# Kernel tuning notes

Hardware: AMD Instinct MI355X
Metric: run time of the kernel (lower is better)

The kernel has to match this reference:

```python
import jax, jax.numpy as jnp
import numpy as np

T, IN_SZ, OUT_SZ = 512, 1024, 1024
INIT_TAU = 2.0   # sig_tau = sigmoid(init_tau) is the leak factor
V_TH = 1.0


def setup_inputs() -> dict:
    key = jax.random.key(0)
    k1, k2 = jax.random.split(key)
    x_seq = jax.random.normal(k1, (T, IN_SZ), jnp.float32)
    kernel = jax.random.normal(k2, (IN_SZ, OUT_SZ), jnp.float32) / np.float32(np.sqrt(IN_SZ))
    u0 = jnp.zeros((OUT_SZ,), jnp.float32)
    E0 = jnp.zeros((IN_SZ, OUT_SZ), jnp.float32)  # eligibility trace, same shape as kernel
    return {"x_seq": x_seq, "kernel": kernel, "u0": u0, "E0": E0}


def reference(x_seq, kernel, u0, E0):
    # Forward pass of the OSTL-wrapped spiking cell over a sequence.
    # Primal path (f): LIF dynamics with soft reset; E is not touched in primal.
    sig_tau = jax.nn.sigmoid(jnp.float32(INIT_TAU))
    vth = jnp.float32(V_TH)

    def body(u, x):
        u_new = sig_tau * u + x @ kernel          # [OUT_SZ]
        s = (u_new > vth).astype(x.dtype)          # heaviside spike
        u_out = u_new - s * vth                    # soft reset
        return u_out, s

    u_final, spikes = jax.lax.scan(body, u0, x_seq)  # spikes: [T, OUT_SZ]
    return spikes, u_final
```

## Files before the change

### kernel.cpp

```cpp
#include <hip/hip_runtime.h>


#define T_STEPS 512
#define IN_SZ   1024
#define OUT_SZ  1024

#define BM 32
#define BN 64
#define BK 32

__global__ __launch_bounds__(256) void ostl_gemm_kernel(const float* __restrict__ X,
                                                        const float* __restrict__ W,
                                                        float* __restrict__ Y) {
    __shared__ float As[2][BK][BM + 4];
    __shared__ float Bs[2][BK][BN];

    const int tid = threadIdx.x;
    const int m0 = blockIdx.y * BM;
    const int n0 = blockIdx.x * BN;
    const int tx = tid & 15;
    const int ty = tid >> 4;

    const int ar  = tid >> 3;
    const int akq = (tid & 7) << 2;
    const int bkr = tid >> 4;
    const int bc  = (tid * 4) & 63;

    const float* Arow = &X[(size_t)(m0 + ar) * IN_SZ + akq];
    const float* Bp0  = &W[(size_t)bkr        * OUT_SZ + n0 + bc];
    const float* Bp1  = &W[(size_t)(bkr + 16) * OUT_SZ + n0 + bc];

    float4 aReg, bReg0, bReg1;

    aReg  = *reinterpret_cast<const float4*>(Arow);
    bReg0 = *reinterpret_cast<const float4*>(Bp0);
    bReg1 = *reinterpret_cast<const float4*>(Bp1);
    As[0][akq + 0][ar] = aReg.x;
    As[0][akq + 1][ar] = aReg.y;
    As[0][akq + 2][ar] = aReg.z;
    As[0][akq + 3][ar] = aReg.w;
    *reinterpret_cast<float4*>(&Bs[0][bkr][bc])      = bReg0;
    *reinterpret_cast<float4*>(&Bs[0][bkr + 16][bc]) = bReg1;
    aReg  = *reinterpret_cast<const float4*>(Arow + BK);
    bReg0 = *reinterpret_cast<const float4*>(Bp0 + (size_t)BK * OUT_SZ);
    bReg1 = *reinterpret_cast<const float4*>(Bp1 + (size_t)BK * OUT_SZ);
    __syncthreads();

    float acc[2][4] = {};

    #pragma unroll 1
    for (int it = 0; it < IN_SZ / BK; ++it) {
        const int cur = it & 1;

        float part[2][4] = {};
        #pragma unroll
        for (int k = 0; k < BK; ++k) {
            const float2 a = *reinterpret_cast<const float2*>(&As[cur][k][ty * 2]);
            const float4 b = *reinterpret_cast<const float4*>(&Bs[cur][k][tx * 4]);
            part[0][0] += a.x * b.x; part[0][1] += a.x * b.y;
            part[0][2] += a.x * b.z; part[0][3] += a.x * b.w;
            part[1][0] += a.y * b.x; part[1][1] += a.y * b.y;
            part[1][2] += a.y * b.z; part[1][3] += a.y * b.w;
        }
        #pragma unroll
        for (int i = 0; i < 2; ++i)
            #pragma unroll
            for (int j = 0; j < 4; ++j)
                acc[i][j] += part[i][j];

        if (it < IN_SZ / BK - 1) {
            const int nxt = cur ^ 1;
            As[nxt][akq + 0][ar] = aReg.x;
            As[nxt][akq + 1][ar] = aReg.y;
            As[nxt][akq + 2][ar] = aReg.z;
            As[nxt][akq + 3][ar] = aReg.w;
            *reinterpret_cast<float4*>(&Bs[nxt][bkr][bc])      = bReg0;
            *reinterpret_cast<float4*>(&Bs[nxt][bkr + 16][bc]) = bReg1;
            if (it < IN_SZ / BK - 2) {
                const int k0 = (it + 2) * BK;
                aReg  = *reinterpret_cast<const float4*>(Arow + k0);
                bReg0 = *reinterpret_cast<const float4*>(Bp0 + (size_t)k0 * OUT_SZ);
                bReg1 = *reinterpret_cast<const float4*>(Bp1 + (size_t)k0 * OUT_SZ);
            }
            __syncthreads();
        }
    }

    #pragma unroll
    for (int i = 0; i < 2; ++i) {
        const float4 v = make_float4(acc[i][0], acc[i][1], acc[i][2], acc[i][3]);
        *reinterpret_cast<float4*>(&Y[(size_t)(m0 + ty * 2 + i) * OUT_SZ + n0 + tx * 4]) = v;
    }
}

#define TB 16

__global__ __launch_bounds__(64) void ostl_scan_kernel(const float* __restrict__ u0,
                                                       float* __restrict__ Yspk,
                                                       float* __restrict__ u_final) {
    const int j = blockIdx.x * blockDim.x + threadIdx.x;
    if (j >= OUT_SZ) return;

    const float  sig_f   = (float)0.8807970779778823;
    const double sig_tau = (double)sig_f;

    double u = (double)u0[j];
    float* p = Yspk + j;

    float bA[TB], bB[TB];

    #pragma unroll
    for (int i = 0; i < TB; ++i) bA[i] = p[(size_t)i * OUT_SZ];

    #pragma unroll 1
    for (int blk = 0; blk < T_STEPS / TB; blk += 2) {
        #pragma unroll
        for (int i = 0; i < TB; ++i)
            bB[i] = p[(size_t)((blk + 1) * TB + i) * OUT_SZ];

        #pragma unroll
        for (int i = 0; i < TB; ++i) {
            u = fma(sig_tau, u, (double)bA[i]);
            const float s = (u > 1.0) ? 1.0f : 0.0f;
            p[(size_t)(blk * TB + i) * OUT_SZ] = s;
            u -= (double)s;
        }

        if (blk + 2 < T_STEPS / TB) {
            #pragma unroll
            for (int i = 0; i < TB; ++i)
                bA[i] = p[(size_t)((blk + 2) * TB + i) * OUT_SZ];
        }

        #pragma unroll
        for (int i = 0; i < TB; ++i) {
            u = fma(sig_tau, u, (double)bB[i]);
            const float s = (u > 1.0) ? 1.0f : 0.0f;
            p[(size_t)((blk + 1) * TB + i) * OUT_SZ] = s;
            u -= (double)s;
        }
    }
    u_final[j] = (float)u;
}

extern "C" void kernel_launch(void* const* d_in, const int* in_sizes, int n_in,
                              void* d_out, int out_size, void* d_ws, size_t ws_size,
                              hipStream_t stream) {
    const float* x_seq  = (const float*)d_in[0];
    const float* kernel = (const float*)d_in[1];
    const float* u0     = (const float*)d_in[2];

    float* out      = (float*)d_out;
    float* spikes   = out;
    float* u_final  = out + (size_t)T_STEPS * OUT_SZ;

    dim3 gemm_grid(OUT_SZ / BN, T_STEPS / BM);
    ostl_gemm_kernel<<<gemm_grid, dim3(256), 0, stream>>>(x_seq, kernel, spikes);

    ostl_scan_kernel<<<dim3(OUT_SZ / 64), dim3(64), 0, stream>>>(u0, spikes, u_final);
}
```

Before: 116.7 us.

## Use 128x128 split-K GEMM with direct global-to-LDS loads and reduction pass

Replaces the small 32x64 tile GEMM with a 128x128 tile, 8x8 per-thread register micro-tile, split across 8 K-chunks so the grid still fills the GPU. B tiles are loaded directly into LDS with global_load_lds. A separate reduction kernel sums the partials into a workspace buffer, which the scan then reads. This raises arithmetic intensity per LDS load but adds partial-sum traffic (8 x 2 MB) and an extra kernel launch.

```diff
diff --git a/kernel.cpp b/kernel.cpp
--- a/kernel.cpp
+++ b/kernel.cpp
@@ -1,102 +1,144 @@
 #include <hip/hip_runtime.h>
+#include <stdint.h>
 
 
 #define T_STEPS 512
 #define IN_SZ   1024
 #define OUT_SZ  1024
 
-#define BM 32
-#define BN 64
+#define BM 128
+#define BN 128
 #define BK 32
-
-__global__ __launch_bounds__(256) void ostl_gemm_kernel(const float* __restrict__ X,
+#define KSPLIT 8
+#define KCHUNK (IN_SZ / KSPLIT)
+#define NITER  (KCHUNK / BK)
+
+typedef __attribute__((address_space(1))) const void gvoid;
+typedef __attribute__((address_space(3))) void lvoid;
+
+__global__ __launch_bounds__(256) void ostl_gemm_splitk(const float* __restrict__ X,
                                                         const float* __restrict__ W,
-                                                        float* __restrict__ Y) {
-    __shared__ float As[2][BK][BM + 4];
-    __shared__ float Bs[2][BK][BN];
+                                                        float* __restrict__ P) {
+    __shared__ float As[2][BK][BM];
+    __shared__ float Bs[2][BK * BN];
 
     const int tid = threadIdx.x;
-    const int m0 = blockIdx.y * BM;
-    const int n0 = blockIdx.x * BN;
     const int tx = tid & 15;
     const int ty = tid >> 4;
-
-    const int ar  = tid >> 3;
-    const int akq = (tid & 7) << 2;
-    const int bkr = tid >> 4;
-    const int bc  = (tid * 4) & 63;
-
-    const float* Arow = &X[(size_t)(m0 + ar) * IN_SZ + akq];
-    const float* Bp0  = &W[(size_t)bkr        * OUT_SZ + n0 + bc];
-    const float* Bp1  = &W[(size_t)(bkr + 16) * OUT_SZ + n0 + bc];
-
-    float4 aReg, bReg0, bReg1;
-
-    aReg  = *reinterpret_cast<const float4*>(Arow);
-    bReg0 = *reinterpret_cast<const float4*>(Bp0);
-    bReg1 = *reinterpret_cast<const float4*>(Bp1);
-    As[0][akq + 0][ar] = aReg.x;
-    As[0][akq + 1][ar] = aReg.y;
-    As[0][akq + 2][ar] = aReg.z;
-    As[0][akq + 3][ar] = aReg.w;
-    *reinterpret_cast<float4*>(&Bs[0][bkr][bc])      = bReg0;
-    *reinterpret_cast<float4*>(&Bs[0][bkr + 16][bc]) = bReg1;
-    aReg  = *reinterpret_cast<const float4*>(Arow + BK);
-    bReg0 = *reinterpret_cast<const float4*>(Bp0 + (size_t)BK * OUT_SZ);
-    bReg1 = *reinterpret_cast<const float4*>(Bp1 + (size_t)BK * OUT_SZ);
+    const int n0 = blockIdx.x * BN;
+    const int m0 = blockIdx.y * BM;
+    const int kc = blockIdx.z;
+    const int kb = kc * KCHUNK;
+
+    const int am = tid >> 1;
+    const int ak = (tid & 1) * 16;
+    const int wv = tid >> 6;
+    const int ln = tid & 63;
+
+    const float* Arow = X + (size_t)(m0 + am) * IN_SZ + kb + ak;
+
+    float4 areg[4];
+
+    #pragma unroll
+    for (int q = 0; q < 4; ++q)
+        areg[q] = *reinterpret_cast<const float4*>(Arow + q * 4);
+    #pragma unroll
+    for (int j = 0; j < 4; ++j) {
+        const int i = wv * 4 + j;
+        const float* src = W + (size_t)(kb + 2 * i + (ln >> 5)) * OUT_SZ + n0 + (ln & 31) * 4;
+        __builtin_amdgcn_global_load_lds((gvoid*)src, (lvoid*)&Bs[0][i * 256], 16, 0, 0);
+    }
+    {
+        float t[16];
+        #pragma unroll
+        for (int q = 0; q < 4; ++q) *reinterpret_cast<float4*>(&t[q * 4]) = areg[q];
+        #pragma unroll
+        for (int c = 0; c < 16; ++c) As[0][ak + c][am] = t[c];
+    }
     __syncthreads();
 
-    float acc[2][4] = {};
+    float acc[8][8];
+    #pragma unroll
+    for (int r = 0; r < 8; ++r)
+        #pragma unroll
+        for (int c = 0; c < 8; ++c) acc[r][c] = 0.f;
 
     #pragma unroll 1
-    for (int it = 0; it < IN_SZ / BK; ++it) {
+    for (int it = 0; it < NITER; ++it) {
         const int cur = it & 1;
-
-        float part[2][4] = {};
-        #pragma unroll
+        const int nxt = cur ^ 1;
+
+        if (it < NITER - 1) {
+            const int kbase = kb + (it + 1) * BK;
+            #pragma unroll
+            for (int j = 0; j < 4; ++j) {
+                const int i = wv * 4 + j;
+                const float* src = W + (size_t)(kbase + 2 * i + (ln >> 5)) * OUT_SZ + n0 + (ln & 31) * 4;
+                __builtin_amdgcn_global_load_lds((gvoid*)src, (lvoid*)&Bs[nxt][i * 256], 16, 0, 0);
+            }
+            #pragma unroll
+            for (int q = 0; q < 4; ++q)
+                areg[q] = *reinterpret_cast<const float4*>(Arow + (it + 1) * BK + q * 4);
+        }
+
+        #pragma unroll 8
         for (int k = 0; k < BK; ++k) {
-            const float2 a = *reinterpret_cast<const float2*>(&As[cur][k][ty * 2]);
-            const float4 b = *reinterpret_cast<const float4*>(&Bs[cur][k][tx * 4]);
-            part[0][0] += a.x * b.x; part[0][1] += a.x * b.y;
-            part[0][2] += a.x * b.z; part[0][3] += a.x * b.w;
-            part[1][0] += a.y * b.x; part[1][1] += a.y * b.y;
-            part[1][2] += a.y * b.z; part[1][3] += a.y * b.w;
-        }
-        #pragma unroll
-        for (int i = 0; i < 2; ++i)
-            #pragma unroll
-            for (int j = 0; j < 4; ++j)
-                acc[i][j] += part[i][j];
-
-        if (it < IN_SZ / BK - 1) {
-            const int nxt = cur ^ 1;
-            As[nxt][akq + 0][ar] = aReg.x;
-            As[nxt][akq + 1][ar] = aReg.y;
-            As[nxt][akq + 2][ar] = aReg.z;
-            As[nxt][akq + 3][ar] = aReg.w;
-            *reinterpret_cast<float4*>(&Bs[nxt][bkr][bc])      = bReg0;
-            *reinterpret_cast<float4*>(&Bs[nxt][bkr + 16][bc]) = bReg1;
-            if (it < IN_SZ / BK - 2) {
-                const int k0 = (it + 2) * BK;
-                aReg  = *reinterpret_cast<const float4*>(Arow + k0);
-                bReg0 = *reinterpret_cast<const float4*>(Bp0 + (size_t)k0 * OUT_SZ);
-                bReg1 = *reinterpret_cast<const float4*>(Bp1 + (size_t)k0 * OUT_SZ);
-            }
+            const float4 a0 = *reinterpret_cast<const float4*>(&As[cur][k][ty * 8]);
+            const float4 a1 = *reinterpret_cast<const float4*>(&As[cur][k][ty * 8 + 4]);
+            const float4 b0 = *reinterpret_cast<const float4*>(&Bs[cur][k * BN + tx * 4]);
+            const float4 b1 = *reinterpret_cast<const float4*>(&Bs[cur][k * BN + tx * 4 + 64]);
+            const float av[8] = {a0.x, a0.y, a0.z, a0.w, a1.x, a1.y, a1.z, a1.w};
+            const float bv[8] = {b0.x, b0.y, b0.z, b0.w, b1.x, b1.y, b1.z, b1.w};
+            #pragma unroll
+            for (int r = 0; r < 8; ++r)
+                #pragma unroll
+                for (int c = 0; c < 8; ++c)
+                    acc[r][c] = fmaf(av[r], bv[c], acc[r][c]);
+        }
+
+        if (it < NITER - 1) {
+            float t[16];
+            #pragma unroll
+            for (int q = 0; q < 4; ++q) *reinterpret_cast<float4*>(&t[q * 4]) = areg[q];
+            #pragma unroll
+            for (int c = 0; c < 16; ++c) As[nxt][ak + c][am] = t[c];
             __syncthreads();
         }
     }
 
-    #pragma unroll
-    for (int i = 0; i < 2; ++i) {
-        const float4 v = make_float4(acc[i][0], acc[i][1], acc[i][2], acc[i][3]);
-        *reinterpret_cast<float4*>(&Y[(size_t)(m0 + ty * 2 + i) * OUT_SZ + n0 + tx * 4]) = v;
-    }
+    float* Pb = P + (size_t)kc * T_STEPS * OUT_SZ + (size_t)(m0 + ty * 8) * OUT_SZ + n0;
+    #pragma unroll
+    for (int r = 0; r < 8; ++r) {
+        *reinterpret_cast<float4*>(&Pb[(size_t)r * OUT_SZ + tx * 4]) =
+            make_float4(acc[r][0], acc[r][1], acc[r][2], acc[r][3]);
+        *reinterpret_cast<float4*>(&Pb[(size_t)r * OUT_SZ + tx * 4 + 64]) =
+            make_float4(acc[r][4], acc[r][5], acc[r][6], acc[r][7]);
+    }
+}
+
+__device__ inline float4 f4add(float4 a, float4 b) {
+    return make_float4(a.x + b.x, a.y + b.y, a.z + b.z, a.w + b.w);
+}
+
+__global__ __launch_bounds__(256) void ostl_reduce8(const float* __restrict__ P,
+                                                    float* __restrict__ Y) {
+    const size_t idx = ((size_t)blockIdx.x * 256 + threadIdx.x) * 4;
+    float4 s[8];
+    #pragma unroll
+    for (int c = 0; c < 8; ++c)
+        s[c] = *reinterpret_cast<const float4*>(P + (size_t)c * T_STEPS * OUT_SZ + idx);
+    const float4 t0 = f4add(s[0], s[1]);
+    const float4 t1 = f4add(s[2], s[3]);
+    const float4 t2 = f4add(s[4], s[5]);
+    const float4 t3 = f4add(s[6], s[7]);
+    *reinterpret_cast<float4*>(Y + idx) = f4add(f4add(t0, t1), f4add(t2, t3));
 }
 
 #define TB 16
 
 __global__ __launch_bounds__(64) void ostl_scan_kernel(const float* __restrict__ u0,
-                                                       float* __restrict__ Yspk,
+                                                       const float* __restrict__ Yin,
+                                                       float* __restrict__ Sout,
                                                        float* __restrict__ u_final) {
     const int j = blockIdx.x * blockDim.x + threadIdx.x;
     if (j >= OUT_SZ) return;
@@ -105,38 +147,39 @@
     const double sig_tau = (double)sig_f;
 
     double u = (double)u0[j];
-    float* p = Yspk + j;
+    const float* pin = Yin + j;
+    float* pout = Sout + j;
 
     float bA[TB], bB[TB];
 
     #pragma unroll
-    for (int i = 0; i < TB; ++i) bA[i] = p[(size_t)i * OUT_SZ];
+    for (int i = 0; i < TB; ++i) bA[i] = pin[(size_t)i * OUT_SZ];
 
     #pragma unroll 1
     for (int blk = 0; blk < T_STEPS / TB; blk += 2) {
         #pragma unroll
         for (int i = 0; i < TB; ++i)
-            bB[i] = p[(size_t)((blk + 1) * TB + i) * OUT_SZ];
+            bB[i] = pin[(size_t)((blk + 1) * TB + i) * OUT_SZ];
 
         #pragma unroll
         for (int i = 0; i < TB; ++i) {
             u = fma(sig_tau, u, (double)bA[i]);
             const float s = (u > 1.0) ? 1.0f : 0.0f;
-            p[(size_t)(blk * TB + i) * OUT_SZ] = s;
+            pout[(size_t)(blk * TB + i) * OUT_SZ] = s;
             u -= (double)s;
         }
 
         if (blk + 2 < T_STEPS / TB) {
             #pragma unroll
             for (int i = 0; i < TB; ++i)
-                bA[i] = p[(size_t)((blk + 2) * TB + i) * OUT_SZ];
+                bA[i] = pin[(size_t)((blk + 2) * TB + i) * OUT_SZ];
         }
 
         #pragma unroll
         for (int i = 0; i < TB; ++i) {
             u = fma(sig_tau, u, (double)bB[i]);
             const float s = (u > 1.0) ? 1.0f : 0.0f;
-            p[(size_t)((blk + 1) * TB + i) * OUT_SZ] = s;
+            pout[(size_t)((blk + 1) * TB + i) * OUT_SZ] = s;
             u -= (double)s;
         }
     }
@@ -154,8 +197,13 @@
     float* spikes   = out;
     float* u_final  = out + (size_t)T_STEPS * OUT_SZ;
 
-    dim3 gemm_grid(OUT_SZ / BN, T_STEPS / BM);
-    ostl_gemm_kernel<<<gemm_grid, dim3(256), 0, stream>>>(x_seq, kernel, spikes);
-
-    ostl_scan_kernel<<<dim3(OUT_SZ / 64), dim3(64), 0, stream>>>(u0, spikes, u_final);
-}
+    float* partials = (float*)d_ws;
+    float* yb       = partials + (size_t)KSPLIT * T_STEPS * OUT_SZ;
+
+    dim3 ggrid(OUT_SZ / BN, T_STEPS / BM, KSPLIT);
+    ostl_gemm_splitk<<<ggrid, dim3(256), 0, stream>>>(x_seq, kernel, partials);
+
+    ostl_reduce8<<<dim3((T_STEPS * OUT_SZ / 4) / 256), dim3(256), 0, stream>>>(partials, yb);
+
+    ostl_scan_kernel<<<dim3(OUT_SZ / 64), dim3(64), 0, stream>>>(u0, yb, spikes, u_final);
+}
```

Measured after the change: 112.4 us. -3.7%, faster.
